# Performance work log

Hardware: AMD Instinct MI355X
Metric: run time of the kernel (lower is better)

Reference implementation:

```python
import jax, jax.numpy as jnp
import numpy as np

DIM = 1024
NUM_HEADS = 16
HEAD_DIM = DIM // NUM_HEADS
B, T = 2, 2048


def setup_inputs() -> dict:
    key = jax.random.key(0)
    ks = jax.random.split(key, 7)
    x = jax.random.normal(ks[0], (B, T, DIM), dtype=jnp.float32)
    # causal mask, broadcastable over batch and heads
    mask = jnp.tril(jnp.ones((T, T), dtype=bool))[None, None, :, :]
    # rope tables for half rotary angles, tiled to head_dim (cat of two halves)
    pos = jnp.arange(T, dtype=jnp.float32)[:, None]
    inv_freq = 1.0 / (10000.0 ** (jnp.arange(0, HEAD_DIM, 2, dtype=jnp.float32) / HEAD_DIM))
    ang = pos * inv_freq[None, :]                      # [T, hd/2]
    ang = jnp.concatenate([ang, ang], axis=-1)         # [T, hd]
    rope_sin = jnp.sin(ang)[None, None, :, :]
    rope_cos = jnp.cos(ang)[None, None, :, :]
    s = 0.02
    qkv_w = jax.random.normal(ks[1], (DIM, 3 * DIM), dtype=jnp.float32) * s
    qkv_b = jnp.zeros((3 * DIM,), dtype=jnp.float32)
    proj_w = jax.random.normal(ks[2], (DIM, DIM), dtype=jnp.float32) * s
    proj_b = jnp.zeros((DIM,), dtype=jnp.float32)
    return {"x": x, "mask": mask, "rope_sin": rope_sin, "rope_cos": rope_cos,
            "qkv_w": qkv_w, "qkv_b": qkv_b, "proj_w": proj_w, "proj_b": proj_b}


def _rotate_half(t):
    half = t.shape[-1] // 2
    return jnp.concatenate([-t[..., half:], t[..., :half]], axis=-1)


def _apply_rope(t, sin, cos):
    return t * cos + _rotate_half(t) * sin


def reference(x, mask, rope_sin, rope_cos, qkv_w, qkv_b, proj_w, proj_b):
    Bb, Tt, C = x.shape
    qkv = x @ qkv_w + qkv_b                            # [B, T, 3C]
    q, k, v = jnp.split(qkv, 3, axis=-1)
    def split_heads(t):                                # [B, T, C] -> [B, H, T, hd]
        return t.reshape(Bb, Tt, NUM_HEADS, HEAD_DIM).transpose(0, 2, 1, 3)
    q, k, v = split_heads(q), split_heads(k), split_heads(v)
    sin = rope_sin[:, :, :Tt, :]
    cos = rope_cos[:, :, :Tt, :]
    q = _apply_rope(q, sin, cos)
    k = _apply_rope(k, sin, cos)
    att = jnp.einsum("bhqd,bhkd->bhqk", q, k) / (HEAD_DIM ** 0.5)
    att = jnp.where(mask, att, -jnp.inf)
    att = jax.nn.softmax(att, axis=-1)
    y = jnp.einsum("bhqk,bhkd->bhqd", att, v)          # [B, H, T, hd]
    y = y.transpose(0, 2, 1, 3).reshape(Bb, Tt, C)
    return y @ proj_w + proj_b
```

## Files before the change

### kernel.cpp

```cpp
#include <hip/hip_runtime.h>

typedef unsigned short u16;
typedef u16 u16x8 __attribute__((ext_vector_type(8)));
typedef __bf16 bf16x8 __attribute__((ext_vector_type(8)));
typedef float f32x4 __attribute__((ext_vector_type(4)));

#define T_SEQ 2048
#define DIM 1024
#define NH 16
#define HD 64

#define MFMA(a, b, c) __builtin_amdgcn_mfma_f32_16x16x32_bf16(a, b, c, 0, 0, 0)

__device__ __forceinline__ u16 f2bf(float f) {
  unsigned u = __builtin_bit_cast(unsigned, f);
  u = u + 0x7fffu + ((u >> 16) & 1u);
  return (u16)(u >> 16);
}

__device__ __forceinline__ bf16x8 ld8(const u16* p) {
  return __builtin_bit_cast(bf16x8, *(const u16x8*)p);
}

__device__ __forceinline__ void gload_lds16(const u16* g, u16* l) {
  __builtin_amdgcn_global_load_lds((const __attribute__((address_space(1))) void*)(g),
                                   (__attribute__((address_space(3))) void*)(l),
                                   16, 0, 0);
}

__global__ void k_prep(const float* __restrict__ X, u16* __restrict__ Y,
                       const float* __restrict__ Wq, u16* __restrict__ WqT,
                       const float* __restrict__ Wp, u16* __restrict__ WpT) {
  __shared__ float tile[32][33];
  int bid = blockIdx.x;
  if (bid < 4096) {
    int i = (bid * 256 + threadIdx.x) * 4;
    float4 f = *(const float4*)&X[i];
    ushort4 o = make_ushort4(f2bf(f.x), f2bf(f.y), f2bf(f.z), f2bf(f.w));
    *(ushort4*)&Y[i] = o;
    return;
  }
  const float* W; u16* WT; int K = 1024, N, bx, by;
  if (bid < 4096 + 3072) { int t = bid - 4096; W = Wq; WT = WqT; N = 3072; bx = t % 96; by = t / 96; }
  else                   { int t = bid - 7168; W = Wp; WT = WpT; N = 1024; bx = t % 32; by = t / 32; }
  int tx = threadIdx.x & 31, ty = threadIdx.x >> 5;
  int c0 = bx * 32, r0 = by * 32;
#pragma unroll
  for (int r = 0; r < 4; r++)
    tile[ty + r * 8][tx] = W[(r0 + ty + r * 8) * N + c0 + tx];
  __syncthreads();
#pragma unroll
  for (int r = 0; r < 4; r++)
    WT[(c0 + ty + r * 8) * K + r0 + tx] = f2bf(tile[tx][ty + r * 8]);
}


#define GEMM_CORE(Aptr, BTptr, Kdim, bxv, byv)                                    \
  const int tid = threadIdx.x;                                                    \
  const int lane = tid & 63, w = tid >> 6;                                        \
  const int l15 = lane & 15, quad = lane >> 4;                                    \
  const int wm = w >> 1, wn = w & 1;                                              \
  const int rowBase = (byv) * 128;                                                \
  const int colBase = (bxv) * 128;                                                \
  f32x4 acc[4][4];                                                                \
  _Pragma("unroll") for (int i = 0; i < 4; i++)                                   \
      _Pragma("unroll") for (int j = 0; j < 4; j++)                               \
          acc[i][j] = (f32x4){0.f, 0.f, 0.f, 0.f};                                \
  const int srow = lane >> 2;                 \
  const int schunk = (lane & 3) * 8;    \
  for (int k0 = 0; k0 < (Kdim); k0 += 32) {                                       \
    __syncthreads();                                                              \
    _Pragma("unroll") for (int p = 0; p < 2; p++) {                               \
      int rr = w * 32 + p * 16;                                                   \
      gload_lds16(&(Aptr)[(size_t)(rowBase + rr + srow) * (Kdim) + k0 + schunk],  \
                  &As[rr * 32]);                                                  \
      gload_lds16(&(BTptr)[(size_t)(colBase + rr + srow) * (Kdim) + k0 + schunk], \
                  &Bs[rr * 32]);                                                  \
    }                                                                             \
    __syncthreads();                 \
    bf16x8 af[4], bfv[4];                                                         \
    _Pragma("unroll") for (int i = 0; i < 4; i++) {                               \
      af[i] = ld8(&As[(wm * 64 + i * 16 + l15) * 32 + quad * 8]);                 \
      bfv[i] = ld8(&Bs[(wn * 64 + i * 16 + l15) * 32 + quad * 8]);                \
    }                                                                             \
    _Pragma("unroll") for (int i = 0; i < 4; i++)                                 \
        _Pragma("unroll") for (int j = 0; j < 4; j++)                             \
            acc[i][j] = MFMA(af[i], bfv[j], acc[i][j]);                           \
  }

__global__ __launch_bounds__(256) void k_gemm_qkv(
    const u16* __restrict__ A, const u16* __restrict__ BT,
    const float* __restrict__ bias,
    const float* __restrict__ rsin, const float* __restrict__ rcos,
    u16* __restrict__ qb, u16* __restrict__ kb, u16* __restrict__ vtb) {
  __shared__ __align__(16) u16 As[128 * 32];
  __shared__ __align__(16) u16 Bs[128 * 32];
  const int n = blockIdx.x, xcd = n & 7, s = n >> 3;
  const int cg = xcd & 1, rg = xcd >> 1;
  const int bxv = cg * 12 + (s >> 3);
  const int byv = rg * 8 + (s & 7);
  GEMM_CORE(A, BT, DIM, bxv, byv)

#pragma unroll
  for (int j = 0; j < 4; j++) {
    float bv = bias[colBase + wn * 64 + j * 16 + l15];
#pragma unroll
    for (int i = 0; i < 4; i++)
#pragma unroll
      for (int r = 0; r < 4; r++) acc[i][j][r] += bv;
  }

  const int colW = colBase + wn * 64;
  const int sec = colW >> 10;
  const int hh = (colW & 1023) >> 6;

#pragma unroll
  for (int i = 0; i < 4; i++) {
#pragma unroll
    for (int r = 0; r < 4; r++) {
      int grow = rowBase + wm * 64 + i * 16 + quad * 4 + r;
      int b = grow >> 11, t = grow & 2047;
#pragma unroll
      for (int j = 0; j < 4; j++) {
        int d = j * 16 + l15;
        float v = acc[i][j][r];
        if (sec == 2) {
          vtb[((b * NH + hh) * HD + d) * T_SEQ + t] = f2bf(v);
        } else {
          float pr = acc[i][j ^ 2][r];
          float rot = (j < 2) ? -pr : pr;
          float rv = v * rcos[t * HD + d] + rot * rsin[t * HD + d];
          if (sec == 0)
            qb[((b * NH + hh) * T_SEQ + t) * HD + d] = f2bf(rv * 0.125f);
          else
            kb[((b * NH + hh) * T_SEQ + t) * HD + d] = f2bf(rv);
        }
      }
    }
  }
}

__global__ __launch_bounds__(256) void k_gemm_proj(
    const u16* __restrict__ A, const u16* __restrict__ BT,
    const float* __restrict__ bias, float* __restrict__ C) {
  __shared__ __align__(16) u16 As[128 * 32];
  __shared__ __align__(16) u16 Bs[128 * 32];
  const int n = blockIdx.x, xcd = n & 7, s = n >> 3;
  const int cg = xcd & 1, rg = xcd >> 1;
  const int bxv = cg * 4 + (s >> 3);
  const int byv = rg * 8 + (s & 7);
  GEMM_CORE(A, BT, DIM, bxv, byv)

#pragma unroll
  for (int i = 0; i < 4; i++)
#pragma unroll
    for (int r = 0; r < 4; r++) {
      int grow = rowBase + wm * 64 + i * 16 + quad * 4 + r;
#pragma unroll
      for (int j = 0; j < 4; j++) {
        int col = colBase + wn * 64 + j * 16 + l15;
        C[grow * DIM + col] = acc[i][j][r] + bias[col];
      }
    }
}

#define KLD 72
#define VLD 136

__global__ __launch_bounds__(256) void k_attn(
    const u16* __restrict__ qb, const u16* __restrict__ kb,
    const u16* __restrict__ vtb, u16* __restrict__ yb) {
  __shared__ __align__(16) u16 Qs[64 * KLD];
  __shared__ __align__(16) u16 Ks[128 * KLD];
  __shared__ __align__(16) u16 VTs[64 * VLD];
  __shared__ __align__(16) u16 Ps[4][16 * VLD];
  const int tid = threadIdx.x;
  const int lane = tid & 63, w = tid >> 6;
  const int l15 = lane & 15, quad = lane >> 4;
  const int bh = blockIdx.x;
  const int qt = 31 - blockIdx.y;

  const u16* qp = qb + (size_t)bh * T_SEQ * HD;
  const u16* kp = kb + (size_t)bh * T_SEQ * HD;
  const u16* vp = vtb + (size_t)bh * HD * T_SEQ;

  {
    int sr = tid >> 3, sc = (tid & 7) * 8;
#pragma unroll
    for (int p = 0; p < 2; p++) {
      int r = sr + p * 32;
      *(u16x8*)&Qs[r * KLD + sc] = *(const u16x8*)&qp[(qt * 64 + r) * HD + sc];
    }
  }
  __syncthreads();
  bf16x8 qa0 = ld8(&Qs[(w * 16 + l15) * KLD + quad * 8]);
  bf16x8 qa1 = ld8(&Qs[(w * 16 + l15) * KLD + 32 + quad * 8]);

  f32x4 o[4];
#pragma unroll
  for (int j = 0; j < 4; j++) o[j] = (f32x4){0.f, 0.f, 0.f, 0.f};
  float li[4] = {0.f, 0.f, 0.f, 0.f};

  const int nch = (qt + 2) >> 1;
  const int qrow_base = qt * 64 + w * 16 + quad * 4;

  for (int c = 0; c < nch; c++) {
    {
      int sr = tid >> 3, sc = (tid & 7) * 8;
#pragma unroll
      for (int p = 0; p < 4; p++) {
        int r = sr + p * 32;
        *(u16x8*)&Ks[r * KLD + sc] = *(const u16x8*)&kp[(c * 128 + r) * HD + sc];
      }
      int vr = tid >> 4, vc = (tid & 15) * 8;
#pragma unroll
      for (int p = 0; p < 4; p++) {
        int r = vr + p * 16;
        *(u16x8*)&VTs[r * VLD + vc] = *(const u16x8*)&vp[r * T_SEQ + c * 128 + vc];
      }
    }
    __syncthreads();

    f32x4 s[8];
#pragma unroll
    for (int j = 0; j < 8; j++) {
      s[j] = (f32x4){0.f, 0.f, 0.f, 0.f};
      bf16x8 b0 = ld8(&Ks[(j * 16 + l15) * KLD + quad * 8]);
      bf16x8 b1 = ld8(&Ks[(j * 16 + l15) * KLD + 32 + quad * 8]);
      s[j] = MFMA(qa0, b0, s[j]);
      s[j] = MFMA(qa1, b1, s[j]);
    }

    u16* ps = &Ps[w][0];
    const bool lastc = (c == nch - 1);
#pragma unroll
    for (int r = 0; r < 4; r++) {
#pragma unroll
      for (int j = 0; j < 8; j++) {
        float e = __expf(s[j][r]);
        if (lastc && (c * 128 + j * 16 + l15 > qrow_base + r)) e = 0.f;
        li[r] += e;
        ps[(quad * 4 + r) * VLD + j * 16 + l15] = f2bf(e);
      }
    }

#pragma unroll
    for (int c4 = 0; c4 < 4; c4++) {
      bf16x8 pa = ld8(&ps[l15 * VLD + c4 * 32 + quad * 8]);
#pragma unroll
      for (int j2 = 0; j2 < 4; j2++) {
        bf16x8 vb = ld8(&VTs[(j2 * 16 + l15) * VLD + c4 * 32 + quad * 8]);
        o[j2] = MFMA(pa, vb, o[j2]);
      }
    }
    __syncthreads();
  }

#pragma unroll
  for (int r = 0; r < 4; r++) {
#pragma unroll
    for (int off = 8; off >= 1; off >>= 1) li[r] += __shfl_xor(li[r], off, 16);
    li[r] = 1.0f / li[r];
  }

  const int b = bh >> 4, h = bh & 15;
#pragma unroll
  for (int j = 0; j < 4; j++)
#pragma unroll
    for (int r = 0; r < 4; r++) {
      int t = qt * 64 + w * 16 + quad * 4 + r;
      int d = j * 16 + l15;
      yb[((b * T_SEQ + t) * NH + h) * HD + d] = f2bf(o[j][r] * li[r]);
    }
}

extern "C" void kernel_launch(void* const* d_in, const int* in_sizes, int n_in,
                              void* d_out, int out_size, void* d_ws, size_t ws_size,
                              hipStream_t stream) {
  const float* x      = (const float*)d_in[0];
  const float* rsin   = (const float*)d_in[2];
  const float* rcos   = (const float*)d_in[3];
  const float* qkv_w  = (const float*)d_in[4];
  const float* qkv_b  = (const float*)d_in[5];
  const float* proj_w = (const float*)d_in[6];
  const float* proj_b = (const float*)d_in[7];
  float* out = (float*)d_out;

  char* ws = (char*)d_ws;
  u16* x_bf  = (u16*)(ws);
  u16* qkvT  = (u16*)(ws + (8ull << 20));
  u16* projT = (u16*)(ws + (14ull << 20));
  u16* q_buf = (u16*)(ws + (16ull << 20));
  u16* k_buf = (u16*)(ws + (24ull << 20));
  u16* vT    = (u16*)(ws + (32ull << 20));
  u16* y_buf = (u16*)(ws + (40ull << 20));

  hipLaunchKernelGGL(k_prep, dim3(8192), dim3(256), 0, stream,
                     x, x_bf, qkv_w, qkvT, proj_w, projT);
  hipLaunchKernelGGL(k_gemm_qkv, dim3(768), dim3(256), 0, stream,
                     x_bf, qkvT, qkv_b, rsin, rcos, q_buf, k_buf, vT);
  hipLaunchKernelGGL(k_attn, dim3(32, 32), dim3(256), 0, stream,
                     q_buf, k_buf, vT, y_buf);
  hipLaunchKernelGGL(k_gemm_proj, dim3(256), dim3(256), 0, stream,
                     y_buf, projT, proj_b, out);
}
```

Baseline: 219.8 us.

## Restructure attention to 128-row query tiles reading K/V directly from global

The attention kernel now gives each block 128 query rows (32 per wave), so each K/V fragment feeds two MFMA row tiles. The K and V^T tiles are no longer staged through shared memory with block-wide barriers; each wave loads its operands straight from global memory, and only the per-wave P buffer stays in LDS. The grid becomes a 1D launch of 512 blocks, remapped so heads are grouped per XCD for L2 locality, and causal chunks align to 128-row tiles. The trade-off is more global/L2 traffic per wave and fewer blocks (less parallelism and coarser causal load balance) in exchange for register reuse and no synchronization.

```diff
diff --git a/kernel.cpp b/kernel.cpp
--- a/kernel.cpp
+++ b/kernel.cpp
@@ -164,114 +164,98 @@
     }
 }
 
-#define KLD 72
-#define VLD 136
+#define PLD 136
 
 __global__ __launch_bounds__(256) void k_attn(
     const u16* __restrict__ qb, const u16* __restrict__ kb,
     const u16* __restrict__ vtb, u16* __restrict__ yb) {
-  __shared__ __align__(16) u16 Qs[64 * KLD];
-  __shared__ __align__(16) u16 Ks[128 * KLD];
-  __shared__ __align__(16) u16 VTs[64 * VLD];
-  __shared__ __align__(16) u16 Ps[4][16 * VLD];
+  __shared__ __align__(16) u16 Ps[4][32 * PLD];
   const int tid = threadIdx.x;
   const int lane = tid & 63, w = tid >> 6;
   const int l15 = lane & 15, quad = lane >> 4;
-  const int bh = blockIdx.x;
-  const int qt = 31 - blockIdx.y;
+  const int n = blockIdx.x, xcd = n & 7, s = n >> 3;
+  const int bh = xcd * 4 + (s & 3);
+  const int qt = 15 - (s >> 2);
 
   const u16* qp = qb + (size_t)bh * T_SEQ * HD;
   const u16* kp = kb + (size_t)bh * T_SEQ * HD;
   const u16* vp = vtb + (size_t)bh * HD * T_SEQ;
 
-  {
-    int sr = tid >> 3, sc = (tid & 7) * 8;
-#pragma unroll
-    for (int p = 0; p < 2; p++) {
-      int r = sr + p * 32;
-      *(u16x8*)&Qs[r * KLD + sc] = *(const u16x8*)&qp[(qt * 64 + r) * HD + sc];
-    }
-  }
-  __syncthreads();
-  bf16x8 qa0 = ld8(&Qs[(w * 16 + l15) * KLD + quad * 8]);
-  bf16x8 qa1 = ld8(&Qs[(w * 16 + l15) * KLD + 32 + quad * 8]);
-
-  f32x4 o[4];
-#pragma unroll
-  for (int j = 0; j < 4; j++) o[j] = (f32x4){0.f, 0.f, 0.f, 0.f};
-  float li[4] = {0.f, 0.f, 0.f, 0.f};
-
-  const int nch = (qt + 2) >> 1;
-  const int qrow_base = qt * 64 + w * 16 + quad * 4;
-
-  for (int c = 0; c < nch; c++) {
-    {
-      int sr = tid >> 3, sc = (tid & 7) * 8;
-#pragma unroll
-      for (int p = 0; p < 4; p++) {
-        int r = sr + p * 32;
-        *(u16x8*)&Ks[r * KLD + sc] = *(const u16x8*)&kp[(c * 128 + r) * HD + sc];
-      }
-      int vr = tid >> 4, vc = (tid & 15) * 8;
-#pragma unroll
-      for (int p = 0; p < 4; p++) {
-        int r = vr + p * 16;
-        *(u16x8*)&VTs[r * VLD + vc] = *(const u16x8*)&vp[r * T_SEQ + c * 128 + vc];
-      }
-    }
-    __syncthreads();
-
-    f32x4 s[8];
+  const int qrow0 = qt * 128 + w * 32;
+  const f32x4 zf = {0.f, 0.f, 0.f, 0.f};
+
+  bf16x8 qa[2][2];
+#pragma unroll
+  for (int t = 0; t < 2; t++)
+#pragma unroll
+    for (int h = 0; h < 2; h++)
+      qa[t][h] = ld8(&qp[(size_t)(qrow0 + t * 16 + l15) * HD + h * 32 + quad * 8]);
+
+  f32x4 o[2][4];
+#pragma unroll
+  for (int t = 0; t < 2; t++)
+#pragma unroll
+    for (int j = 0; j < 4; j++) o[t][j] = zf;
+  f32x4 li[2] = {zf, zf};
+
+  u16* ps = &Ps[w][0];
+  const int wq = w * 32 + quad * 4;
+
+  for (int c = 0; c <= qt; c++) {
+    const bool dia = (c == qt);
+    const int kbase = c * 128;
 #pragma unroll
     for (int j = 0; j < 8; j++) {
-      s[j] = (f32x4){0.f, 0.f, 0.f, 0.f};
-      bf16x8 b0 = ld8(&Ks[(j * 16 + l15) * KLD + quad * 8]);
-      bf16x8 b1 = ld8(&Ks[(j * 16 + l15) * KLD + 32 + quad * 8]);
-      s[j] = MFMA(qa0, b0, s[j]);
-      s[j] = MFMA(qa1, b1, s[j]);
-    }
-
-    u16* ps = &Ps[w][0];
-    const bool lastc = (c == nch - 1);
+      const u16* kr = &kp[(size_t)(kbase + j * 16 + l15) * HD + quad * 8];
+      bf16x8 b0 = ld8(kr);
+      bf16x8 b1 = ld8(kr + 32);
+#pragma unroll
+      for (int t = 0; t < 2; t++) {
+        f32x4 s0 = MFMA(qa[t][0], b0, zf);
+        f32x4 sv = MFMA(qa[t][1], b1, s0);
+#pragma unroll
+        for (int r = 0; r < 4; r++) {
+          float e = __expf(sv[r]);
+          if (dia && (j * 16 + l15 > wq + t * 16 + r)) e = 0.f;
+          li[t][r] += e;
+          ps[(t * 16 + quad * 4 + r) * PLD + j * 16 + l15] = f2bf(e);
+        }
+      }
+    }
+#pragma unroll
+    for (int c4 = 0; c4 < 4; c4++) {
+      bf16x8 pa0 = ld8(&ps[l15 * PLD + c4 * 32 + quad * 8]);
+      bf16x8 pa1 = ld8(&ps[(16 + l15) * PLD + c4 * 32 + quad * 8]);
+#pragma unroll
+      for (int j2 = 0; j2 < 4; j2++) {
+        bf16x8 vb = ld8(&vp[(size_t)(j2 * 16 + l15) * T_SEQ + kbase + c4 * 32 + quad * 8]);
+        o[0][j2] = MFMA(pa0, vb, o[0][j2]);
+        o[1][j2] = MFMA(pa1, vb, o[1][j2]);
+      }
+    }
+  }
+
+#pragma unroll
+  for (int t = 0; t < 2; t++)
 #pragma unroll
     for (int r = 0; r < 4; r++) {
-#pragma unroll
-      for (int j = 0; j < 8; j++) {
-        float e = __expf(s[j][r]);
-        if (lastc && (c * 128 + j * 16 + l15 > qrow_base + r)) e = 0.f;
-        li[r] += e;
-        ps[(quad * 4 + r) * VLD + j * 16 + l15] = f2bf(e);
-      }
-    }
-
-#pragma unroll
-    for (int c4 = 0; c4 < 4; c4++) {
-      bf16x8 pa = ld8(&ps[l15 * VLD + c4 * 32 + quad * 8]);
-#pragma unroll
-      for (int j2 = 0; j2 < 4; j2++) {
-        bf16x8 vb = ld8(&VTs[(j2 * 16 + l15) * VLD + c4 * 32 + quad * 8]);
-        o[j2] = MFMA(pa, vb, o[j2]);
-      }
-    }
-    __syncthreads();
-  }
-
-#pragma unroll
-  for (int r = 0; r < 4; r++) {
-#pragma unroll
-    for (int off = 8; off >= 1; off >>= 1) li[r] += __shfl_xor(li[r], off, 16);
-    li[r] = 1.0f / li[r];
-  }
+      float v = li[t][r];
+#pragma unroll
+      for (int off = 8; off >= 1; off >>= 1) v += __shfl_xor(v, off, 16);
+      li[t][r] = 1.0f / v;
+    }
 
   const int b = bh >> 4, h = bh & 15;
 #pragma unroll
-  for (int j = 0; j < 4; j++)
-#pragma unroll
-    for (int r = 0; r < 4; r++) {
-      int t = qt * 64 + w * 16 + quad * 4 + r;
-      int d = j * 16 + l15;
-      yb[((b * T_SEQ + t) * NH + h) * HD + d] = f2bf(o[j][r] * li[r]);
-    }
+  for (int t = 0; t < 2; t++)
+#pragma unroll
+    for (int j2 = 0; j2 < 4; j2++)
+#pragma unroll
+      for (int r = 0; r < 4; r++) {
+        int trow = qrow0 + t * 16 + quad * 4 + r;
+        int d = j2 * 16 + l15;
+        yb[((b * T_SEQ + trow) * NH + h) * HD + d] = f2bf(o[t][j2][r] * li[t][r]);
+      }
 }
 
 extern "C" void kernel_launch(void* const* d_in, const int* in_sizes, int n_in,
@@ -299,7 +283,7 @@
                      x, x_bf, qkv_w, qkvT, proj_w, projT);
   hipLaunchKernelGGL(k_gemm_qkv, dim3(768), dim3(256), 0, stream,
                      x_bf, qkvT, qkv_b, rsin, rcos, q_buf, k_buf, vT);
-  hipLaunchKernelGGL(k_attn, dim3(32, 32), dim3(256), 0, stream,
+  hipLaunchKernelGGL(k_attn, dim3(512), dim3(256), 0, stream,
                      q_buf, k_buf, vT, y_buf);
   hipLaunchKernelGGL(k_gemm_proj, dim3(256), dim3(256), 0, stream,
                      y_buf, projT, proj_b, out);
```

Measured after the change: 296.5 us. 34.9% more time.

## Permute V key order to vectorize P stores; load Q directly to registers

Applied to the files above, without the earlier changes.

The QKV epilogue now writes V^T with the key index permuted inside each 128-key block, so that each lane's 8 softmax probabilities (one per j-tile) become contiguous. P can then be written to LDS as one 16-byte store instead of eight scalar stores. The P·V product stays correct because P and V^T share the same permuted key order. Q fragments are now read straight from global memory into registers, which drops the Q LDS staging and one barrier. The weight-transpose prep also writes four bf16 values per store.

```diff
diff --git a/kernel.cpp b/kernel.cpp
--- a/kernel.cpp
+++ b/kernel.cpp
@@ -49,9 +49,10 @@
   for (int r = 0; r < 4; r++)
     tile[ty + r * 8][tx] = W[(r0 + ty + r * 8) * N + c0 + tx];
   __syncthreads();
-#pragma unroll
-  for (int r = 0; r < 4; r++)
-    WT[(c0 + ty + r * 8) * K + r0 + tx] = f2bf(tile[tx][ty + r * 8]);
+  int n_l = threadIdx.x >> 3, kg = (threadIdx.x & 7) * 4;
+  ushort4 ov = make_ushort4(f2bf(tile[kg + 0][n_l]), f2bf(tile[kg + 1][n_l]),
+                            f2bf(tile[kg + 2][n_l]), f2bf(tile[kg + 3][n_l]));
+  *(ushort4*)&WT[(size_t)(c0 + n_l) * K + r0 + kg] = ov;
 }
 
 
@@ -125,7 +126,8 @@
         int d = j * 16 + l15;
         float v = acc[i][j][r];
         if (sec == 2) {
-          vtb[((b * NH + hh) * HD + d) * T_SEQ + t] = f2bf(v);
+          int tp = (t & ~127) | (((t & 15) << 3) | ((t >> 4) & 7));
+          vtb[((b * NH + hh) * HD + d) * T_SEQ + tp] = f2bf(v);
         } else {
           float pr = acc[i][j ^ 2][r];
           float rot = (j < 2) ? -pr : pr;
@@ -166,14 +168,14 @@
 
 #define KLD 72
 #define VLD 136
+#define PLD 136
 
 __global__ __launch_bounds__(256) void k_attn(
     const u16* __restrict__ qb, const u16* __restrict__ kb,
     const u16* __restrict__ vtb, u16* __restrict__ yb) {
-  __shared__ __align__(16) u16 Qs[64 * KLD];
   __shared__ __align__(16) u16 Ks[128 * KLD];
   __shared__ __align__(16) u16 VTs[64 * VLD];
-  __shared__ __align__(16) u16 Ps[4][16 * VLD];
+  __shared__ __align__(16) u16 Ps[4][16 * PLD];
   const int tid = threadIdx.x;
   const int lane = tid & 63, w = tid >> 6;
   const int l15 = lane & 15, quad = lane >> 4;
@@ -184,17 +186,9 @@
   const u16* kp = kb + (size_t)bh * T_SEQ * HD;
   const u16* vp = vtb + (size_t)bh * HD * T_SEQ;
 
-  {
-    int sr = tid >> 3, sc = (tid & 7) * 8;
-#pragma unroll
-    for (int p = 0; p < 2; p++) {
-      int r = sr + p * 32;
-      *(u16x8*)&Qs[r * KLD + sc] = *(const u16x8*)&qp[(qt * 64 + r) * HD + sc];
-    }
-  }
-  __syncthreads();
-  bf16x8 qa0 = ld8(&Qs[(w * 16 + l15) * KLD + quad * 8]);
-  bf16x8 qa1 = ld8(&Qs[(w * 16 + l15) * KLD + 32 + quad * 8]);
+  const int qrow16 = qt * 64 + w * 16;
+  bf16x8 qa0 = ld8(&qp[(size_t)(qrow16 + l15) * HD + quad * 8]);
+  bf16x8 qa1 = ld8(&qp[(size_t)(qrow16 + l15) * HD + 32 + quad * 8]);
 
   f32x4 o[4];
 #pragma unroll
@@ -203,6 +197,7 @@
 
   const int nch = (qt + 2) >> 1;
   const int qrow_base = qt * 64 + w * 16 + quad * 4;
+  u16* ps = &Ps[w][0];
 
   for (int c = 0; c < nch; c++) {
     {
@@ -210,13 +205,13 @@
 #pragma unroll
       for (int p = 0; p < 4; p++) {
         int r = sr + p * 32;
-        *(u16x8*)&Ks[r * KLD + sc] = *(const u16x8*)&kp[(c * 128 + r) * HD + sc];
+        *(u16x8*)&Ks[r * KLD + sc] = *(const u16x8*)&kp[(size_t)(c * 128 + r) * HD + sc];
       }
       int vr = tid >> 4, vc = (tid & 15) * 8;
 #pragma unroll
       for (int p = 0; p < 4; p++) {
         int r = vr + p * 16;
-        *(u16x8*)&VTs[r * VLD + vc] = *(const u16x8*)&vp[r * T_SEQ + c * 128 + vc];
+        *(u16x8*)&VTs[r * VLD + vc] = *(const u16x8*)&vp[(size_t)r * T_SEQ + c * 128 + vc];
       }
     }
     __syncthreads();
@@ -231,22 +226,23 @@
       s[j] = MFMA(qa1, b1, s[j]);
     }
 
-    u16* ps = &Ps[w][0];
     const bool lastc = (c == nch - 1);
 #pragma unroll
     for (int r = 0; r < 4; r++) {
+      u16x8 pk;
 #pragma unroll
       for (int j = 0; j < 8; j++) {
         float e = __expf(s[j][r]);
         if (lastc && (c * 128 + j * 16 + l15 > qrow_base + r)) e = 0.f;
         li[r] += e;
-        ps[(quad * 4 + r) * VLD + j * 16 + l15] = f2bf(e);
-      }
+        pk[j] = f2bf(e);
+      }
+      *(u16x8*)&ps[(quad * 4 + r) * PLD + l15 * 8] = pk;
     }
 
 #pragma unroll
     for (int c4 = 0; c4 < 4; c4++) {
-      bf16x8 pa = ld8(&ps[l15 * VLD + c4 * 32 + quad * 8]);
+      bf16x8 pa = ld8(&ps[l15 * PLD + c4 * 32 + quad * 8]);
 #pragma unroll
       for (int j2 = 0; j2 < 4; j2++) {
         bf16x8 vb = ld8(&VTs[(j2 * 16 + l15) * VLD + c4 * 32 + quad * 8]);
```

Measured after the change: 261.8 us. 1.19x slower.
